# Kernel optimization log

Hardware: AMD Instinct MI355X
Metric: run time of the kernel (lower is better)

## Reference

```python
import jax, jax.numpy as jnp
import numpy as np

B, K, DIM = 8192, 256, 1024


def setup_inputs() -> dict:
    key = jax.random.key(0)
    k1, k2, k3 = jax.random.split(key, 3)
    x = jax.random.normal(k1, (B, DIM), dtype=jnp.float32)
    centers = jax.random.uniform(k2, (K, DIM), dtype=jnp.float32)
    # torch init: D = 0.2 * rand + 0.9
    D = 0.2 * jax.random.uniform(k3, (K, DIM), dtype=jnp.float32) + 0.9
    return {"x": x, "centers": centers, "D": D}


def reference(x, centers, D):
    # Per-class axis-aligned (diagonal) covariance
    D_abs = jnp.abs(D) + 1e-4                      # [K, DIM]
    D_inv = 1.0 / D_abs                            # [K, DIM]
    log_det = jnp.sum(jnp.log(D_abs), axis=1)      # [K]
    det_scale_factor = -0.5 * log_det
    det_scale_safe = jnp.exp(det_scale_factor - jnp.max(det_scale_factor))  # [K]

    # dist_sq[b,k] = sum_d (x[b,d]-c[k,d])^2 * D_inv[k,d]
    # Expanded quadratic form avoids materializing the [B,K,DIM] diff tensor.
    x2 = jnp.einsum('bd,kd->bk', x * x, D_inv)             # [B, K]
    xc = jnp.einsum('bd,kd->bk', x, centers * D_inv)       # [B, K]
    c2 = jnp.sum(centers * centers * D_inv, axis=1)        # [K]
    dist_sq = x2 - 2.0 * xc + c2[None, :]                  # [B, K]

    # Gaussian path (isCauchy=False)
    expo = -0.5 * dist_sq
    expo_safe = expo - jnp.max(expo, axis=-1, keepdims=True)
    numer_safe = det_scale_safe[None, :] * jnp.exp(expo_safe)
    denom_safe = jnp.sum(numer_safe, axis=1, keepdims=True)
    resp = numer_safe / denom_safe                         # [B, K]
    return resp
```

## Files before the change

kernel.cpp:

```cpp
#include <hip/hip_runtime.h>

typedef _Float16 f16x8 __attribute__((ext_vector_type(8)));
typedef _Float16 f16x4 __attribute__((ext_vector_type(4)));
typedef float f32x4 __attribute__((ext_vector_type(4)));

#define B_N 8192
#define K_N 256
#define DIM_N 1024

__global__ __launch_bounds__(256) void prep_w(const float* __restrict__ Dm,
                                              const float* __restrict__ Cm,
                                              _Float16* __restrict__ Uf,
                                              _Float16* __restrict__ Wf,
                                              float* __restrict__ ec) {
    const int k = blockIdx.x, t = threadIdx.x;
    const int d = t * 4;
    const float4 dv = *(const float4*)(Dm + (size_t)k * DIM_N + d);
    const float4 cv = *(const float4*)(Cm + (size_t)k * DIM_N + d);
    float dd[4] = {dv.x, dv.y, dv.z, dv.w};
    float cc[4] = {cv.x, cv.y, cv.z, cv.w};
    f16x4 uo, wo;
    float llog = 0.f, lc2 = 0.f;
#pragma unroll
    for (int i = 0; i < 4; ++i) {
        float da = fabsf(dd[i]) + 1e-4f;
        float dinv = 1.0f / da;
        llog += logf(da);
        lc2 += cc[i] * cc[i] * dinv;
        uo[i] = (_Float16)(dinv - 1.0f);
        wo[i] = (_Float16)(-2.0f * cc[i] * dinv);
    }
    *(f16x4*)(Uf + (size_t)k * DIM_N + d) = uo;
    *(f16x4*)(Wf + (size_t)k * DIM_N + d) = wo;
    float both = llog + lc2;
#pragma unroll
    for (int m = 1; m <= 32; m <<= 1) both += __shfl_xor(both, m, 64);
    __shared__ float sb[4];
    if ((t & 63) == 0) sb[t >> 6] = both;
    __syncthreads();
    if (t == 0) ec[k] = -0.5f * (sb[0] + sb[1] + sb[2] + sb[3]);
}

__global__ __launch_bounds__(512, 1)
void gmm_gemm(const float* __restrict__ x,
              const _Float16* __restrict__ Uf,
              const _Float16* __restrict__ Wf,
              float* __restrict__ S) {
    __shared__ __align__(16) char lds[98304];

    const int tid = threadIdx.x;
    const int wave = tid >> 6, lane = tid & 63, l15 = lane & 15, g = lane >> 4;
    const int wr = wave >> 2, wc = wave & 3;

    const int bid = blockIdx.x;
    const int xcd = bid & 7, idx = bid >> 3;
    const int colp = idx & 1;
    const int rowp = (idx >> 1) * 8 + xcd;
    const int bRow = rowp * 64;
    const int bCol = colp * 128;

    const int xrow = tid >> 3, xs = tid & 7;
    const float* xp = x + (size_t)(bRow + xrow) * DIM_N + xs * 8;
    const int aWr = xs * 1024 + (((xrow ^ xs) & 63) << 4);
    const int wrow = tid >> 2, wq = tid & 3;
    const _Float16* up = Uf + (size_t)(bCol + wrow) * DIM_N + wq * 16;
    const _Float16* wp = Wf + (size_t)(bCol + wrow) * DIM_N + wq * 16;
    int bWr[2];
#pragma unroll
    for (int j = 0; j < 2; ++j) {
        const int s = wq * 2 + j;
        bWr[j] = s * 2048 + (((wrow ^ s) & 127) << 4);
    }

    int aRd[2][2], bRd[2][2];
#pragma unroll
    for (int k2 = 0; k2 < 2; ++k2) {
        const int s = k2 * 4 + g;
#pragma unroll
        for (int m = 0; m < 2; ++m) {
            const int row = wr * 32 + m * 16 + l15;
            aRd[m][k2] = s * 1024 + (((row ^ s) & 63) << 4);
        }
#pragma unroll
        for (int n = 0; n < 2; ++n) {
            const int col = wc * 32 + n * 16 + l15;
            bRd[n][k2] = s * 2048 + (((col ^ s) & 127) << 4);
        }
    }

    f32x4 acc[2][2];
#pragma unroll
    for (int m = 0; m < 2; ++m)
#pragma unroll
        for (int n = 0; n < 2; ++n) {
            f32x4 z = {0.f, 0.f, 0.f, 0.f};
            acc[m][n] = z;
        }

    float4 xv[2][2];
    f16x8 uv[2][2], wv[2][2];

    auto loadX = [&](int bank, int c) {
        xv[bank][0] = *(const float4*)(xp + c * 64);
        xv[bank][1] = *(const float4*)(xp + c * 64 + 4);
    };
    auto loadW = [&](int bank, int c) {
        uv[bank][0] = *(const f16x8*)(up + c * 64);
        uv[bank][1] = *(const f16x8*)(up + c * 64 + 8);
        wv[bank][0] = *(const f16x8*)(wp + c * 64);
        wv[bank][1] = *(const f16x8*)(wp + c * 64 + 8);
    };
    auto stage = [&](int base, int bank) {
        float f[8] = {xv[bank][0].x, xv[bank][0].y, xv[bank][0].z, xv[bank][0].w,
                      xv[bank][1].x, xv[bank][1].y, xv[bank][1].z, xv[bank][1].w};
        _Float16 h2[8], hx[8];
#pragma unroll
        for (int i = 0; i < 8; ++i) {
            h2[i] = (_Float16)(f[i] * f[i]);
            hx[i] = (_Float16)f[i];
        }
        *(f16x8*)(lds + base + aWr) = *(const f16x8*)&h2[0];
        *(f16x8*)(lds + base + 8192 + aWr) = *(const f16x8*)&hx[0];
        *(f16x8*)(lds + base + 16384 + bWr[0]) = uv[bank][0];
        *(f16x8*)(lds + base + 16384 + bWr[1]) = uv[bank][1];
        *(f16x8*)(lds + base + 32768 + bWr[0]) = wv[bank][0];
        *(f16x8*)(lds + base + 32768 + bWr[1]) = wv[bank][1];
    };

    loadX(0, 0); loadW(0, 0);
    loadX(1, 1); loadW(1, 1);
    stage(0, 0);
    asm volatile("s_waitcnt lgkmcnt(0)" ::: "memory");
    __builtin_amdgcn_s_barrier();
    __builtin_amdgcn_sched_barrier(0);

#pragma unroll
    for (int c = 0; c < 16; ++c) {
        const int cur = c & 1, nxt = cur ^ 1;
        const int bCur = cur * 49152, bNxt = nxt * 49152;
        if (c < 14) { loadX(cur, c + 2); loadW(cur, c + 2); }
        f16x8 a2f[2][2], axf[2][2], buf[2][2], bwf[2][2];
#pragma unroll
        for (int k2 = 0; k2 < 2; ++k2) {
#pragma unroll
            for (int m = 0; m < 2; ++m) {
                a2f[m][k2] = *(const f16x8*)(lds + bCur + aRd[m][k2]);
                axf[m][k2] = *(const f16x8*)(lds + bCur + 8192 + aRd[m][k2]);
            }
#pragma unroll
            for (int n = 0; n < 2; ++n) {
                buf[n][k2] = *(const f16x8*)(lds + bCur + 16384 + bRd[n][k2]);
                bwf[n][k2] = *(const f16x8*)(lds + bCur + 32768 + bRd[n][k2]);
            }
        }
        __builtin_amdgcn_s_setprio(1);
#pragma unroll
        for (int m = 0; m < 2; ++m)
#pragma unroll
            for (int n = 0; n < 2; ++n)
#pragma unroll
                for (int k2 = 0; k2 < 2; ++k2) {
                    acc[m][n] = __builtin_amdgcn_mfma_f32_16x16x32_f16(a2f[m][k2], buf[n][k2], acc[m][n], 0, 0, 0);
                    acc[m][n] = __builtin_amdgcn_mfma_f32_16x16x32_f16(axf[m][k2], bwf[n][k2], acc[m][n], 0, 0, 0);
                }
        __builtin_amdgcn_s_setprio(0);
        if (c < 15) {
            stage(bNxt, nxt);
            asm volatile("s_waitcnt lgkmcnt(0)" ::: "memory");
            __builtin_amdgcn_s_barrier();
            __builtin_amdgcn_sched_barrier(0);
        }
    }

#pragma unroll
    for (int m = 0; m < 2; ++m) {
        const int rb = bRow + wr * 32 + m * 16 + g * 4;
        const int cb = bCol + wc * 32 + l15;
#pragma unroll
        for (int j = 0; j < 4; ++j) {
            float* p = S + (size_t)(rb + j) * K_N + cb;
            p[0] = acc[m][0][j];
            p[16] = acc[m][1][j];
        }
    }
}

__global__ __launch_bounds__(256)
void gmm_soft(float* __restrict__ S, const float* __restrict__ ecg) {
    const int tid = threadIdx.x;
    const int wave = tid >> 6, lane = tid & 63;
    const int r = blockIdx.x * 4 + wave;
    const int k0 = lane * 4;
    float4 s = *(const float4*)(S + (size_t)r * K_N + k0);
    float4 cv = *(const float4*)(ecg + k0);
    float e[4] = {fmaf(-0.5f, s.x, cv.x), fmaf(-0.5f, s.y, cv.y),
                  fmaf(-0.5f, s.z, cv.z), fmaf(-0.5f, s.w, cv.w)};
    float m = fmaxf(fmaxf(e[0], e[1]), fmaxf(e[2], e[3]));
#pragma unroll
    for (int msk = 1; msk <= 32; msk <<= 1) m = fmaxf(m, __shfl_xor(m, msk, 64));
    float p[4], sum = 0.f;
#pragma unroll
    for (int j = 0; j < 4; ++j) {
        p[j] = __expf(e[j] - m);
        sum += p[j];
    }
#pragma unroll
    for (int msk = 1; msk <= 32; msk <<= 1) sum += __shfl_xor(sum, msk, 64);
    const float inv = 1.0f / sum;
    *(float4*)(S + (size_t)r * K_N + k0) = make_float4(p[0] * inv, p[1] * inv, p[2] * inv, p[3] * inv);
}

extern "C" void kernel_launch(void* const* d_in, const int* in_sizes, int n_in,
                              void* d_out, int out_size, void* d_ws, size_t ws_size,
                              hipStream_t stream) {
    const float* x = (const float*)d_in[0];
    const float* cen = (const float*)d_in[1];
    const float* Dm = (const float*)d_in[2];
    float* out = (float*)d_out;

    char* ws = (char*)d_ws;
    _Float16* Uf = (_Float16*)(ws);
    _Float16* Wf = (_Float16*)(ws + 524288);
    float* ec = (float*)(ws + 1048576);

    prep_w<<<dim3(K_N), dim3(256), 0, stream>>>(Dm, cen, Uf, Wf, ec);
    gmm_gemm<<<dim3(256), dim3(512), 0, stream>>>(x, Uf, Wf, out);
    gmm_soft<<<dim3(B_N / 4), dim3(256), 0, stream>>>(out, ec);
}
```

Baseline: 36.05 us.

## Pre-pack weights in MFMA fragment layout and load B directly to registers

The prep kernel now writes the U and W half-precision weights in a fragment-packed layout, so each GEMM wave can load its B operands straight from global memory into registers without going through LDS. The GEMM moves to 256 threads with 4 waves, each covering a 32x64 tile. Each wave stages only its own x tile in a private LDS region, which removes all block-wide barriers. The K chunk shrinks to 32, with triple-buffered x prefetch and double-buffered B registers. The aim is to cut LDS traffic and synchronisation, at the cost of more global loads per wave (no B sharing across the two row waves), more registers, and half as many waves per CU.

```diff
diff --git a/kernel.cpp b/kernel.cpp
--- a/kernel.cpp
+++ b/kernel.cpp
@@ -10,8 +10,8 @@
 
 __global__ __launch_bounds__(256) void prep_w(const float* __restrict__ Dm,
                                               const float* __restrict__ Cm,
-                                              _Float16* __restrict__ Uf,
-                                              _Float16* __restrict__ Wf,
+                                              _Float16* __restrict__ Upk,
+                                              _Float16* __restrict__ Wpk,
                                               float* __restrict__ ec) {
     const int k = blockIdx.x, t = threadIdx.x;
     const int d = t * 4;
@@ -30,8 +30,11 @@
         uo[i] = (_Float16)(dinv - 1.0f);
         wo[i] = (_Float16)(-2.0f * cc[i] * dinv);
     }
-    *(f16x4*)(Uf + (size_t)k * DIM_N + d) = uo;
-    *(f16x4*)(Wf + (size_t)k * DIM_N + d) = wo;
+    const int cg = k >> 4, cl = k & 15;
+    const int kc = d >> 5, g = (d >> 3) & 3, j0 = d & 7;
+    const size_t off = ((size_t)(cg * 32 + kc) * 64 + g * 16 + cl) * 8 + j0;
+    *(f16x4*)(Upk + off) = uo;
+    *(f16x4*)(Wpk + off) = wo;
     float both = llog + lc2;
 #pragma unroll
     for (int m = 1; m <= 32; m <<= 1) both += __shfl_xor(both, m, 64);
@@ -41,146 +44,111 @@
     if (t == 0) ec[k] = -0.5f * (sb[0] + sb[1] + sb[2] + sb[3]);
 }
 
-__global__ __launch_bounds__(512, 1)
+__global__ __launch_bounds__(256, 1)
 void gmm_gemm(const float* __restrict__ x,
-              const _Float16* __restrict__ Uf,
-              const _Float16* __restrict__ Wf,
+              const _Float16* __restrict__ Upk,
+              const _Float16* __restrict__ Wpk,
               float* __restrict__ S) {
-    __shared__ __align__(16) char lds[98304];
+    __shared__ __align__(16) char lds[32768];
 
     const int tid = threadIdx.x;
-    const int wave = tid >> 6, lane = tid & 63, l15 = lane & 15, g = lane >> 4;
-    const int wr = wave >> 2, wc = wave & 3;
+    const int wave = tid >> 6, lane = tid & 63;
+    const int l15 = lane & 15, g4 = lane >> 4;
+    const int wr = wave >> 1, wc = wave & 1;
+    const int bid = blockIdx.x;
+    const int rowp = bid >> 1, colp = bid & 1;
+    const int bRow = rowp * 64, bCol = colp * 128;
 
-    const int bid = blockIdx.x;
-    const int xcd = bid & 7, idx = bid >> 3;
-    const int colp = idx & 1;
-    const int rowp = (idx >> 1) * 8 + xcd;
-    const int bRow = rowp * 64;
-    const int bCol = colp * 128;
+    const int xr = lane >> 3, xdq = lane & 7;
+    const float* xp = x + (size_t)(bRow + wr * 32 + xr) * DIM_N + xdq * 4;
 
-    const int xrow = tid >> 3, xs = tid & 7;
-    const float* xp = x + (size_t)(bRow + xrow) * DIM_N + xs * 8;
-    const int aWr = xs * 1024 + (((xrow ^ xs) & 63) << 4);
-    const int wrow = tid >> 2, wq = tid & 3;
-    const _Float16* up = Uf + (size_t)(bCol + wrow) * DIM_N + wq * 16;
-    const _Float16* wp = Wf + (size_t)(bCol + wrow) * DIM_N + wq * 16;
-    int bWr[2];
+    const int cgb = colp * 8 + wc * 4;
+    const _Float16* upb = Upk + (size_t)cgb * 32 * 512 + lane * 8;
+    const _Float16* wpb = Wpk + (size_t)cgb * 32 * 512 + lane * 8;
+
+    char* wlds = lds + wave * 8192;
+    const int di = xdq >> 1, jb = (lane & 1) * 8;
+    int awr[4];
 #pragma unroll
-    for (int j = 0; j < 2; ++j) {
-        const int s = wq * 2 + j;
-        bWr[j] = s * 2048 + (((wrow ^ s) & 127) << 4);
+    for (int i = 0; i < 4; ++i) {
+        const int r = xr + 8 * i;
+        awr[i] = ((r >> 4) << 10) + (((r & 15) + (di << 4)) << 4) + jb;
     }
 
-    int aRd[2][2], bRd[2][2];
-#pragma unroll
-    for (int k2 = 0; k2 < 2; ++k2) {
-        const int s = k2 * 4 + g;
-#pragma unroll
-        for (int m = 0; m < 2; ++m) {
-            const int row = wr * 32 + m * 16 + l15;
-            aRd[m][k2] = s * 1024 + (((row ^ s) & 63) << 4);
-        }
-#pragma unroll
-        for (int n = 0; n < 2; ++n) {
-            const int col = wc * 32 + n * 16 + l15;
-            bRd[n][k2] = s * 2048 + (((col ^ s) & 127) << 4);
-        }
-    }
-
-    f32x4 acc[2][2];
+    float4 xv[3][4];
+    f16x8 ub[2][4], wb[2][4];
+    f32x4 acc[2][4];
 #pragma unroll
     for (int m = 0; m < 2; ++m)
 #pragma unroll
-        for (int n = 0; n < 2; ++n) {
-            f32x4 z = {0.f, 0.f, 0.f, 0.f};
-            acc[m][n] = z;
+        for (int n = 0; n < 4; ++n) { f32x4 z = {0.f, 0.f, 0.f, 0.f}; acc[m][n] = z; }
+
+    auto issueB = [&](int bank, int c) {
+#pragma unroll
+        for (int n = 0; n < 4; ++n) {
+            ub[bank][n] = *(const f16x8*)(upb + ((size_t)n * 32 + c) * 512);
+            wb[bank][n] = *(const f16x8*)(wpb + ((size_t)n * 32 + c) * 512);
         }
-
-    float4 xv[2][2];
-    f16x8 uv[2][2], wv[2][2];
-
-    auto loadX = [&](int bank, int c) {
-        xv[bank][0] = *(const float4*)(xp + c * 64);
-        xv[bank][1] = *(const float4*)(xp + c * 64 + 4);
     };
-    auto loadW = [&](int bank, int c) {
-        uv[bank][0] = *(const f16x8*)(up + c * 64);
-        uv[bank][1] = *(const f16x8*)(up + c * 64 + 8);
-        wv[bank][0] = *(const f16x8*)(wp + c * 64);
-        wv[bank][1] = *(const f16x8*)(wp + c * 64 + 8);
+    auto issueX = [&](int slot, int c) {
+#pragma unroll
+        for (int i = 0; i < 4; ++i)
+            xv[slot][i] = *(const float4*)(xp + (size_t)c * 32 + (size_t)i * 8 * DIM_N);
     };
-    auto stage = [&](int base, int bank) {
-        float f[8] = {xv[bank][0].x, xv[bank][0].y, xv[bank][0].z, xv[bank][0].w,
-                      xv[bank][1].x, xv[bank][1].y, xv[bank][1].z, xv[bank][1].w};
-        _Float16 h2[8], hx[8];
+    auto stageA = [&](int sel, int slot) {
+        char* base = wlds + sel * 4096;
 #pragma unroll
-        for (int i = 0; i < 8; ++i) {
-            h2[i] = (_Float16)(f[i] * f[i]);
-            hx[i] = (_Float16)f[i];
+        for (int i = 0; i < 4; ++i) {
+            const float f0 = xv[slot][i].x, f1 = xv[slot][i].y;
+            const float f2 = xv[slot][i].z, f3 = xv[slot][i].w;
+            f16x4 h2 = {(_Float16)(f0 * f0), (_Float16)(f1 * f1),
+                        (_Float16)(f2 * f2), (_Float16)(f3 * f3)};
+            f16x4 hx = {(_Float16)f0, (_Float16)f1, (_Float16)f2, (_Float16)f3};
+            *(f16x4*)(base + awr[i]) = h2;
+            *(f16x4*)(base + 2048 + awr[i]) = hx;
         }
-        *(f16x8*)(lds + base + aWr) = *(const f16x8*)&h2[0];
-        *(f16x8*)(lds + base + 8192 + aWr) = *(const f16x8*)&hx[0];
-        *(f16x8*)(lds + base + 16384 + bWr[0]) = uv[bank][0];
-        *(f16x8*)(lds + base + 16384 + bWr[1]) = uv[bank][1];
-        *(f16x8*)(lds + base + 32768 + bWr[0]) = wv[bank][0];
-        *(f16x8*)(lds + base + 32768 + bWr[1]) = wv[bank][1];
     };
-
-    loadX(0, 0); loadW(0, 0);
-    loadX(1, 1); loadW(1, 1);
-    stage(0, 0);
-    asm volatile("s_waitcnt lgkmcnt(0)" ::: "memory");
-    __builtin_amdgcn_s_barrier();
-    __builtin_amdgcn_sched_barrier(0);
-
+    auto compute = [&](int sel, int bank) {
+        char* base = wlds + sel * 4096;
+        f16x8 a2f[2], axf[2];
 #pragma unroll
-    for (int c = 0; c < 16; ++c) {
-        const int cur = c & 1, nxt = cur ^ 1;
-        const int bCur = cur * 49152, bNxt = nxt * 49152;
-        if (c < 14) { loadX(cur, c + 2); loadW(cur, c + 2); }
-        f16x8 a2f[2][2], axf[2][2], buf[2][2], bwf[2][2];
-#pragma unroll
-        for (int k2 = 0; k2 < 2; ++k2) {
-#pragma unroll
-            for (int m = 0; m < 2; ++m) {
-                a2f[m][k2] = *(const f16x8*)(lds + bCur + aRd[m][k2]);
-                axf[m][k2] = *(const f16x8*)(lds + bCur + 8192 + aRd[m][k2]);
-            }
-#pragma unroll
-            for (int n = 0; n < 2; ++n) {
-                buf[n][k2] = *(const f16x8*)(lds + bCur + 16384 + bRd[n][k2]);
-                bwf[n][k2] = *(const f16x8*)(lds + bCur + 32768 + bRd[n][k2]);
-            }
+        for (int m = 0; m < 2; ++m) {
+            a2f[m] = *(const f16x8*)(base + m * 1024 + lane * 16);
+            axf[m] = *(const f16x8*)(base + 2048 + m * 1024 + lane * 16);
         }
         __builtin_amdgcn_s_setprio(1);
 #pragma unroll
         for (int m = 0; m < 2; ++m)
 #pragma unroll
-            for (int n = 0; n < 2; ++n)
+            for (int n = 0; n < 4; ++n) {
+                acc[m][n] = __builtin_amdgcn_mfma_f32_16x16x32_f16(a2f[m], ub[bank][n], acc[m][n], 0, 0, 0);
+                acc[m][n] = __builtin_amdgcn_mfma_f32_16x16x32_f16(axf[m], wb[bank][n], acc[m][n], 0, 0, 0);
+            }
+        __builtin_amdgcn_s_setprio(0);
+    };
+
+    issueB(0, 0);
+    issueX(0, 0); issueX(1, 1); issueX(2, 2);
+    stageA(0, 0);
+
 #pragma unroll
-                for (int k2 = 0; k2 < 2; ++k2) {
-                    acc[m][n] = __builtin_amdgcn_mfma_f32_16x16x32_f16(a2f[m][k2], buf[n][k2], acc[m][n], 0, 0, 0);
-                    acc[m][n] = __builtin_amdgcn_mfma_f32_16x16x32_f16(axf[m][k2], bwf[n][k2], acc[m][n], 0, 0, 0);
-                }
-        __builtin_amdgcn_s_setprio(0);
-        if (c < 15) {
-            stage(bNxt, nxt);
-            asm volatile("s_waitcnt lgkmcnt(0)" ::: "memory");
-            __builtin_amdgcn_s_barrier();
-            __builtin_amdgcn_sched_barrier(0);
-        }
+    for (int c = 0; c < 32; ++c) {
+        const int sel = c & 1;
+        if (c < 31) issueB(sel ^ 1, c + 1);
+        if (c < 29) issueX((c + 3) % 3, c + 3);
+        if (c < 31) stageA(sel ^ 1, (c + 1) % 3);
+        compute(sel, sel);
     }
 
 #pragma unroll
     for (int m = 0; m < 2; ++m) {
-        const int rb = bRow + wr * 32 + m * 16 + g * 4;
-        const int cb = bCol + wc * 32 + l15;
+        const int rb = bRow + wr * 32 + m * 16 + g4 * 4;
 #pragma unroll
-        for (int j = 0; j < 4; ++j) {
-            float* p = S + (size_t)(rb + j) * K_N + cb;
-            p[0] = acc[m][0][j];
-            p[16] = acc[m][1][j];
+        for (int n = 0; n < 4; ++n) {
+            const int cb = bCol + wc * 64 + n * 16 + l15;
+#pragma unroll
+            for (int j = 0; j < 4; ++j)
+                S[(size_t)(rb + j) * K_N + cb] = acc[m][n][j];
         }
     }
 }
@@ -219,11 +187,11 @@
     float* out = (float*)d_out;
 
     char* ws = (char*)d_ws;
-    _Float16* Uf = (_Float16*)(ws);
-    _Float16* Wf = (_Float16*)(ws + 524288);
+    _Float16* Upk = (_Float16*)(ws);
+    _Float16* Wpk = (_Float16*)(ws + 524288);
     float* ec = (float*)(ws + 1048576);
 
-    prep_w<<<dim3(K_N), dim3(256), 0, stream>>>(Dm, cen, Uf, Wf, ec);
-    gmm_gemm<<<dim3(256), dim3(512), 0, stream>>>(x, Uf, Wf, out);
+    prep_w<<<dim3(K_N), dim3(256), 0, stream>>>(Dm, cen, Upk, Wpk, ec);
+    gmm_gemm<<<dim3(256), dim3(256), 0, stream>>>(x, Upk, Wpk, out);
     gmm_soft<<<dim3(B_N / 4), dim3(256), 0, stream>>>(out, ec);
 }
```

After: 36.25 us. About the same (+0.6%).
